# Performance work log

Hardware: AMD Instinct MI355X
Metric: run time of the kernel (lower is better)

Reference implementation:

```python
import jax, jax.numpy as jnp
import numpy as np

B, D_IN, HD, HN = 16384, 1024, 128, 8
D = HD * HN  # 1024
PROJ = int((4.0 / 3.0) * D)  # 1365
EPS = 1e-5


def setup_inputs() -> dict:
    key = jax.random.key(0)
    ks = jax.random.split(key, 16)
    s = 0.02
    inp = {
        'seq': jax.random.normal(ks[0], (B, D_IN), jnp.float32),
        'c0': jnp.zeros((B, D), jnp.float32),
        'n0': jnp.ones((B, D), jnp.float32),
        'h0': jax.random.normal(ks[1], (B, D), jnp.float32) * 0.1,
        'm0': jnp.zeros((B, D), jnp.float32),
        'ln_w': jnp.ones((D_IN,), jnp.float32),
        'ln_b': jnp.zeros((D_IN,), jnp.float32),
        'Wz': jax.random.normal(ks[2], (D, D_IN), jnp.float32) * s,
        'bz': jnp.zeros((D,), jnp.float32),
        'Wi': jax.random.normal(ks[3], (D, D_IN), jnp.float32) * s,
        'bi': jnp.zeros((D,), jnp.float32),
        'Wo': jax.random.normal(ks[4], (D, D_IN), jnp.float32) * s,
        'bo': jnp.zeros((D,), jnp.float32),
        'Wf': jax.random.normal(ks[5], (D, D_IN), jnp.float32) * s,
        'bf': jnp.zeros((D,), jnp.float32),
        'Rz': jax.random.normal(ks[6], (HN, HD, HD), jnp.float32) * s,
        'Ri': jax.random.normal(ks[7], (HN, HD, HD), jnp.float32) * s,
        'Ro': jax.random.normal(ks[8], (HN, HD, HD), jnp.float32) * s,
        'Rf': jax.random.normal(ks[9], (HN, HD, HD), jnp.float32) * s,
        'gn_w': jnp.ones((D,), jnp.float32),
        'gn_b': jnp.zeros((D,), jnp.float32),
        'up_w': jax.random.normal(ks[10], (2 * PROJ, D), jnp.float32) * s,
        'up_b': jnp.zeros((2 * PROJ,), jnp.float32),
        'down_w': jax.random.normal(ks[11], (D_IN, PROJ), jnp.float32) * s,
        'down_b': jnp.zeros((D_IN,), jnp.float32),
    }
    return inp


def _layernorm(x, w, b):
    mu = jnp.mean(x, axis=-1, keepdims=True)
    var = jnp.mean(jnp.square(x - mu), axis=-1, keepdims=True)
    return (x - mu) * jax.lax.rsqrt(var + EPS) * w + b


def _groupnorm(x, w, b):
    # x: (B, D) -> groups of HD channels per head
    xr = x.reshape(x.shape[0], HN, HD)
    mu = jnp.mean(xr, axis=-1, keepdims=True)
    var = jnp.mean(jnp.square(xr - mu), axis=-1, keepdims=True)
    xn = ((xr - mu) * jax.lax.rsqrt(var + EPS)).reshape(x.shape)
    return xn * w + b


def _block_linear(h, R):
    # block-diagonal recurrence: per-head (HD,HD) matmul
    hr = h.reshape(h.shape[0], HN, HD)
    return jnp.einsum('hed,bhd->bhe', R, hr).reshape(h.shape)


def reference(seq, c0, n0, h0, m0, ln_w, ln_b, Wz, bz, Wi, bi, Wo, bo, Wf, bf,
              Rz, Ri, Ro, Rf, gn_w, gn_b, up_w, up_b, down_w, down_b):
    x_t = _layernorm(seq, ln_w, ln_b)
    x_c = x_t  # use_conv=False default path
    i_t = x_c @ Wi.T + bi + _block_linear(h0, Ri)
    f_t = x_c @ Wf.T + bf + _block_linear(h0, Rf)
    z_t = x_t @ Wz.T + bz + _block_linear(h0, Rz)
    o_t = x_t @ Wo.T + bo + _block_linear(h0, Ro)
    m_t = jnp.maximum(f_t + m0, i_t)
    i_e = jnp.exp(i_t - m_t)
    f_e = jnp.exp(f_t - m_t + m0)
    z_a = jnp.tanh(z_t)
    o_a = jax.nn.sigmoid(o_t)
    c_t = f_e * c0 + i_e * z_a
    n_t = f_e * n0 + i_e
    h_t = o_a * (c_t / n_t)
    out = _groupnorm(h_t, gn_w, gn_b)
    up = out @ up_w.T + up_b
    out1, out2 = jnp.split(up, 2, axis=-1)
    out = out1 + jax.nn.gelu(out2, approximate=False)
    out = out @ down_w.T + down_b
    return (out + seq, c_t, n_t, h_t, m_t)
```

## Files before the change

### kernel.cpp

```cpp
#include <hip/hip_runtime.h>
#include <hip/hip_bf16.h>
#include <cstdint>
#include <type_traits>

typedef __attribute__((ext_vector_type(8))) __bf16 bf16x8;
typedef __attribute__((ext_vector_type(8))) short short8;
typedef __attribute__((ext_vector_type(4))) float f32x4;
using u16 = unsigned short;

template <typename T, typename = void> struct mfma_ok : std::false_type {};
template <typename T>
struct mfma_ok<T, std::void_t<decltype(__builtin_amdgcn_mfma_f32_16x16x32_bf16(
    std::declval<T>(), std::declval<T>(), std::declval<f32x4>(), 0, 0, 0))>>
    : std::true_type {};
using frag_t = std::conditional_t<mfma_ok<bf16x8>::value, bf16x8, short8>;
static_assert(sizeof(frag_t) == 16, "frag must be 4 VGPRs");

template <typename T>
__device__ __forceinline__ f32x4 MFMA(T a, T b, f32x4 c) {
  return __builtin_amdgcn_mfma_f32_16x16x32_bf16(a, b, c, 0, 0, 0);
}

__device__ __forceinline__ void gl_lds16(const u16* g, u16* l) {
  __builtin_amdgcn_global_load_lds(
      (const __attribute__((address_space(1))) unsigned int*)g,
      (__attribute__((address_space(3))) unsigned int*)l, 16, 0, 0);
}

__device__ __forceinline__ u16 f2bf(float v) {
  __hip_bfloat16 h = __float2bfloat16(v);
  return __builtin_bit_cast(u16, h);
}

__device__ __forceinline__ int xcd_swz(int wid, int nwg) {
  return (wid & 7) * (nwg >> 3) + (wid >> 3);
}

__device__ __forceinline__ void gemm128(
    const u16* __restrict__ A, int lda,
    const u16* __restrict__ B, int ldb, int K,
    u16* lds, f32x4 (&acc)[4][4])
{
  const int t = threadIdx.x;
  const int l = t & 63;
  const int w = t >> 6;
  const int wm = w >> 1, wc = w & 1;

  const u16* gA = A + (t >> 2) * lda + (t & 3) * 8;
  const u16* gB = B + (t >> 2) * ldb + (t & 3) * 8;

  const int lr = l & 15, lk = l >> 4;
  const int ab = (wm * 64 + lr) * 32 + lk * 8;
  const int bb = 4096 + (wc * 64 + lr) * 32 + lk * 8;

  const int nt = K >> 5;
  for (int kt = 0; kt < nt; ++kt) {
    const u16* a_ = gA + kt * 32;
    const u16* b_ = gB + kt * 32;
    gl_lds16(a_,            lds + w * 512);
    gl_lds16(a_ + 64 * lda, lds + 2048 + w * 512);
    gl_lds16(b_,            lds + 4096 + w * 512);
    gl_lds16(b_ + 64 * ldb, lds + 6144 + w * 512);
    __syncthreads();

    frag_t a[4], b[4];
#pragma unroll
    for (int fm = 0; fm < 4; ++fm)
      a[fm] = *(const frag_t*)(lds + ab + fm * 512);
#pragma unroll
    for (int fn = 0; fn < 4; ++fn)
      b[fn] = *(const frag_t*)(lds + bb + fn * 512);
#pragma unroll
    for (int fn = 0; fn < 4; ++fn)
#pragma unroll
      for (int fm = 0; fm < 4; ++fm)
        acc[fm][fn] = MFMA(a[fm], b[fn], acc[fm][fn]);
    __syncthreads();
  }
}

__global__ __launch_bounds__(256) void prep_kernel(
    const float* __restrict__ Wi, const float* __restrict__ Wf,
    const float* __restrict__ Wz, const float* __restrict__ Wo,
    const float* __restrict__ Ri, const float* __restrict__ Rf,
    const float* __restrict__ Rz, const float* __restrict__ Ro,
    const float* __restrict__ upw, const float* __restrict__ dnw,
    u16* __restrict__ Wint, u16* __restrict__ Rint,
    u16* __restrict__ upint, u16* __restrict__ dnp)
{
  const int stride = gridDim.x * 256;
  for (int i = blockIdx.x * 256 + threadIdx.x; i < 9043968; i += stride) {
    if (i < 4194304) {
      const int nt = i >> 17, vcol = (i >> 10) & 127, k = i & 1023;
      const int wc = vcol >> 6, g = (vcol >> 4) & 3, c16 = vcol & 15;
      const int col = nt * 32 + wc * 16 + c16;
      const float* W = (g == 0) ? Wi : (g == 1) ? Wf : (g == 2) ? Wz : Wo;
      Wint[i] = f2bf(W[col * 1024 + k]);
    } else if (i < 4718592) {
      const int j = i - 4194304;
      const int nt = j >> 14, vcol = (j >> 7) & 127, k = j & 127;
      const int wc = vcol >> 6, g = (vcol >> 4) & 3, c16 = vcol & 15;
      const int head = nt >> 2;
      const int colInHead = (nt & 3) * 32 + wc * 16 + c16;
      const float* R = (g == 0) ? Ri : (g == 1) ? Rf : (g == 2) ? Rz : Ro;
      Rint[j] = f2bf(R[head * 16384 + colInHead * 128 + k]);
    } else if (i < 7602176) {
      const int j = i - 4718592;
      const int vt = j >> 17, vcol = (j >> 10) & 127, k = j & 1023;
      const int wc = vcol >> 6, fn = (vcol >> 4) & 3, c16 = vcol & 15;
      const int half = fn >> 1;
      const int a = vt * 64 + wc * 32 + (fn & 1) * 16 + c16;
      upint[j] = (a < 1365) ? f2bf(upw[(half * 1365 + a) * 1024 + k]) : (u16)0;
    } else {
      const int j = i - 7602176;
      const int row = j / 1408, k = j - row * 1408;
      dnp[j] = (k < 1365) ? f2bf(dnw[row * 1365 + k]) : (u16)0;
    }
  }
}

__global__ __launch_bounds__(256) void ln_kernel(
    const float* __restrict__ seq, const float* __restrict__ h0,
    const float* __restrict__ lnw, const float* __restrict__ lnb,
    u16* __restrict__ xb, u16* __restrict__ h0b)
{
  const int row = blockIdx.x;
  const int t = threadIdx.x;
  const float4 v = ((const float4*)(seq + (size_t)row * 1024))[t];
  float s = v.x + v.y + v.z + v.w;
  float q = v.x * v.x + v.y * v.y + v.z * v.z + v.w * v.w;
#pragma unroll
  for (int o = 32; o >= 1; o >>= 1) { s += __shfl_xor(s, o); q += __shfl_xor(q, o); }
  __shared__ float sm[8];
  const int l = t & 63, w = t >> 6;
  if (l == 0) { sm[w] = s; sm[4 + w] = q; }
  __syncthreads();
  s = sm[0] + sm[1] + sm[2] + sm[3];
  q = sm[4] + sm[5] + sm[6] + sm[7];
  const float mu = s * (1.f / 1024.f);
  const float var = q * (1.f / 1024.f) - mu * mu;
  const float rstd = rsqrtf(var + 1e-5f);
  const float4 wv = ((const float4*)lnw)[t];
  const float4 bv = ((const float4*)lnb)[t];
  ushort4 o4;
  o4.x = f2bf((v.x - mu) * rstd * wv.x + bv.x);
  o4.y = f2bf((v.y - mu) * rstd * wv.y + bv.y);
  o4.z = f2bf((v.z - mu) * rstd * wv.z + bv.z);
  o4.w = f2bf((v.w - mu) * rstd * wv.w + bv.w);
  ((ushort4*)(xb + (size_t)row * 1024))[t] = o4;
  const float4 h = ((const float4*)(h0 + (size_t)row * 1024))[t];
  ushort4 h4;
  h4.x = f2bf(h.x); h4.y = f2bf(h.y); h4.z = f2bf(h.z); h4.w = f2bf(h.w);
  ((ushort4*)(h0b + (size_t)row * 1024))[t] = h4;
}

__global__ __launch_bounds__(256, 3) void gate_kernel(
    const u16* __restrict__ xb, const u16* __restrict__ h0b,
    const u16* __restrict__ Wint, const u16* __restrict__ Rint,
    const float* __restrict__ bi, const float* __restrict__ bfv,
    const float* __restrict__ bz, const float* __restrict__ bo,
    const float* __restrict__ c0, const float* __restrict__ n0i,
    const float* __restrict__ m0,
    float* __restrict__ oc, float* __restrict__ on,
    float* __restrict__ oh, float* __restrict__ om)
{
  __shared__ __align__(16) u16 lds[8192];
  const int wid = xcd_swz(blockIdx.x, 4096);
  const int nt = wid & 31;
  const int mt = wid >> 5;
  f32x4 acc[4][4] = {};
  gemm128(xb + (size_t)mt * 131072, 1024, Wint + nt * 131072, 1024, 1024,
          lds, acc);
  gemm128(h0b + (size_t)mt * 131072 + (nt >> 2) * 128, 1024,
          Rint + nt * 16384, 128, 128, lds, acc);

  const int t = threadIdx.x, l = t & 63, w = t >> 6, wm = w >> 1, wc = w & 1;
  const int cc = nt * 32 + wc * 16 + (l & 15);
  const float biv = bi[cc], bfvv = bfv[cc], bzv = bz[cc], bov = bo[cc];
#pragma unroll
  for (int fm = 0; fm < 4; ++fm) {
    const int rbase = mt * 128 + wm * 64 + fm * 16 + (l >> 4) * 4;
#pragma unroll
    for (int r = 0; r < 4; ++r) {
      const size_t idx = (size_t)(rbase + r) * 1024 + cc;
      const float it = acc[fm][0][r] + biv;
      const float ft = acc[fm][1][r] + bfvv;
      const float zt = acc[fm][2][r] + bzv;
      const float ot = acc[fm][3][r] + bov;
      const float mp = m0[idx];
      const float mt_ = fmaxf(ft + mp, it);
      const float ie = __expf(it - mt_);
      const float fe = __expf(ft - mt_ + mp);
      const float ct = fe * c0[idx] + ie * tanhf(zt);
      const float ntv = fe * n0i[idx] + ie;
      const float ht = (ct / ntv) / (1.f + __expf(-ot));
      oc[idx] = ct; on[idx] = ntv; oh[idx] = ht; om[idx] = mt_;
    }
  }
}

__global__ __launch_bounds__(256) void gn_kernel(
    const float* __restrict__ h, const float* __restrict__ gw,
    const float* __restrict__ gb, u16* __restrict__ gnb)
{
  const int t = threadIdx.x, l = t & 63, w = t >> 6;
  for (int grp = blockIdx.x * 4 + w; grp < 16384 * 8; grp += gridDim.x * 4) {
    const int b = grp >> 3, hd = grp & 7;
    const float2 v = ((const float2*)(h + b * 1024 + hd * 128))[l];
    float s = v.x + v.y, q = v.x * v.x + v.y * v.y;
#pragma unroll
    for (int o = 32; o >= 1; o >>= 1) { s += __shfl_xor(s, o); q += __shfl_xor(q, o); }
    const float mu = s * (1.f / 128.f);
    const float var = q * (1.f / 128.f) - mu * mu;
    const float rstd = rsqrtf(var + 1e-5f);
    const float2 wv = ((const float2*)(gw + hd * 128))[l];
    const float2 bv = ((const float2*)(gb + hd * 128))[l];
    ushort2 o2;
    o2.x = f2bf((v.x - mu) * rstd * wv.x + bv.x);
    o2.y = f2bf((v.y - mu) * rstd * wv.y + bv.y);
    ((ushort2*)(gnb + b * 1024 + hd * 128))[l] = o2;
  }
}

__global__ __launch_bounds__(256, 3) void up_kernel(
    const u16* __restrict__ gnb, const u16* __restrict__ upint,
    const float* __restrict__ upb, u16* __restrict__ g)
{
  __shared__ __align__(16) u16 lds[8192];
  const int wid = xcd_swz(blockIdx.x, 2816);
  const int vt = wid % 22, mt = wid / 22;
  f32x4 acc[4][4] = {};
  gemm128(gnb + (size_t)mt * 131072, 1024, upint + vt * 131072, 1024, 1024,
          lds, acc);
  const int t = threadIdx.x, l = t & 63, w = t >> 6, wm = w >> 1, wc = w & 1;
#pragma unroll
  for (int fm = 0; fm < 4; ++fm) {
    const int rbase = mt * 128 + wm * 64 + fm * 16 + (l >> 4) * 4;
#pragma unroll
    for (int fn = 0; fn < 2; ++fn) {
      const int a = vt * 64 + wc * 32 + fn * 16 + (l & 15);
      const float b1 = (a < 1365) ? upb[a] : 0.f;
      const float b2 = (a < 1365) ? upb[1365 + a] : 0.f;
#pragma unroll
      for (int r = 0; r < 4; ++r) {
        const float u1 = acc[fm][fn][r] + b1;
        const float u2 = acc[fm][fn + 2][r] + b2;
        const float ge = 0.5f * u2 * (1.f + erff(u2 * 0.70710678118654752f));
        g[(size_t)(rbase + r) * 1408 + a] = f2bf(u1 + ge);
      }
    }
  }
}

__global__ __launch_bounds__(256, 3) void down_kernel(
    const u16* __restrict__ g, const u16* __restrict__ dnp,
    const float* __restrict__ dnb, const float* __restrict__ seq,
    float* __restrict__ out)
{
  __shared__ __align__(16) u16 lds[8192];
  const int wid = xcd_swz(blockIdx.x, 1024);
  const int nt = wid & 7, mt = wid >> 3;
  f32x4 acc[4][4] = {};
  gemm128(g + (size_t)mt * 180224, 1408, dnp + nt * 180224, 1408, 1408,
          lds, acc);
  const int t = threadIdx.x, l = t & 63, w = t >> 6, wm = w >> 1, wc = w & 1;
#pragma unroll
  for (int fm = 0; fm < 4; ++fm) {
    const int rbase = mt * 128 + wm * 64 + fm * 16 + (l >> 4) * 4;
#pragma unroll
    for (int fn = 0; fn < 4; ++fn) {
      const int cc = nt * 128 + wc * 64 + fn * 16 + (l & 15);
      const float bb = dnb[cc];
#pragma unroll
      for (int r = 0; r < 4; ++r) {
        const size_t idx = (size_t)(rbase + r) * 1024 + cc;
        out[idx] = acc[fm][fn][r] + bb + seq[idx];
      }
    }
  }
}

extern "C" void kernel_launch(void* const* d_in, const int* in_sizes, int n_in,
                              void* d_out, int out_size, void* d_ws, size_t ws_size,
                              hipStream_t stream) {
  const float* seq = (const float*)d_in[0];
  const float* c0  = (const float*)d_in[1];
  const float* n0i = (const float*)d_in[2];
  const float* h0  = (const float*)d_in[3];
  const float* m0  = (const float*)d_in[4];
  const float* lnw = (const float*)d_in[5];
  const float* lnb = (const float*)d_in[6];
  const float* Wz  = (const float*)d_in[7];
  const float* bz  = (const float*)d_in[8];
  const float* Wi  = (const float*)d_in[9];
  const float* bi  = (const float*)d_in[10];
  const float* Wo  = (const float*)d_in[11];
  const float* bo  = (const float*)d_in[12];
  const float* Wf  = (const float*)d_in[13];
  const float* bf_ = (const float*)d_in[14];
  const float* Rz  = (const float*)d_in[15];
  const float* Ri  = (const float*)d_in[16];
  const float* Ro  = (const float*)d_in[17];
  const float* Rf  = (const float*)d_in[18];
  const float* gw  = (const float*)d_in[19];
  const float* gb  = (const float*)d_in[20];
  const float* upw = (const float*)d_in[21];
  const float* upb = (const float*)d_in[22];
  const float* dnw = (const float*)d_in[23];
  const float* dnb = (const float*)d_in[24];

  char* ws = (char*)d_ws;
  u16* xb   = (u16*)(ws);
  u16* h0b  = (u16*)(ws + 33554432);
  u16* Wint = (u16*)(ws + 67108864);
  u16* Rint = (u16*)(ws + 75497472);
  u16* upc  = (u16*)(ws + 76546048);
  u16* dnp  = (u16*)(ws + 82313216);
  u16* g    = (u16*)(ws + 85196800);

  float* out = (float*)d_out;
  float* oc = out + 16777216;
  float* on = out + 2 * 16777216;
  float* oh = out + 3 * 16777216;
  float* om = out + 4 * 16777216;

  prep_kernel<<<dim3(2048), dim3(256), 0, stream>>>(
      Wi, Wf, Wz, Wo, Ri, Rf, Rz, Ro, upw, dnw, Wint, Rint, upc, dnp);
  ln_kernel<<<dim3(16384), dim3(256), 0, stream>>>(seq, h0, lnw, lnb, xb, h0b);
  gate_kernel<<<dim3(4096), dim3(256), 0, stream>>>(
      xb, h0b, Wint, Rint, bi, bf_, bz, bo, c0, n0i, m0, oc, on, oh, om);
  gn_kernel<<<dim3(2048), dim3(256), 0, stream>>>(oh, gw, gb, xb);
  up_kernel<<<dim3(2816), dim3(256), 0, stream>>>(xb, upc, upb, g);
  down_kernel<<<dim3(1024), dim3(256), 0, stream>>>(g, dnp, dnb, seq, out);
}
```

Before: 563.9 us.

## Double-buffer LDS in GEMM mainloop with XOR swizzle to avoid bank conflicts

```diff
diff --git a/kernel.cpp b/kernel.cpp
--- a/kernel.cpp
+++ b/kernel.cpp
@@ -46,37 +46,55 @@
   const int w = t >> 6;
   const int wm = w >> 1, wc = w & 1;
 
-  const u16* gA = A + (t >> 2) * lda + (t & 3) * 8;
-  const u16* gB = B + (t >> 2) * ldb + (t & 3) * 8;
+  const int srow = t >> 2;
+  const int scol = ((t & 3) ^ ((srow >> 1) & 3)) * 8;
+  const u16* gA = A + srow * lda + scol;
+  const u16* gB = B + srow * ldb + scol;
 
   const int lr = l & 15, lk = l >> 4;
-  const int ab = (wm * 64 + lr) * 32 + lk * 8;
-  const int bb = 4096 + (wc * 64 + lr) * 32 + lk * 8;
+  const int ck = (lk ^ ((lr >> 1) & 3)) * 8;
+  const int ab = (wm * 64 + lr) * 32 + ck;
+  const int bb = 4096 + (wc * 64 + lr) * 32 + ck;
 
   const int nt = K >> 5;
+
+#define STG(buf, kt) do {                                      \
+    const u16* a_ = gA + (kt) * 32;                            \
+    const u16* b_ = gB + (kt) * 32;                            \
+    u16* s_ = (buf);                                           \
+    gl_lds16(a_,            s_ + w * 512);                     \
+    gl_lds16(a_ + 64 * lda, s_ + 2048 + w * 512);              \
+    gl_lds16(b_,            s_ + 4096 + w * 512);              \
+    gl_lds16(b_ + 64 * ldb, s_ + 6144 + w * 512);              \
+  } while (0)
+
+  STG(lds, 0);
+  asm volatile("s_waitcnt vmcnt(0)" ::: "memory");
+  __builtin_amdgcn_s_barrier();
+
   for (int kt = 0; kt < nt; ++kt) {
-    const u16* a_ = gA + kt * 32;
-    const u16* b_ = gB + kt * 32;
-    gl_lds16(a_,            lds + w * 512);
-    gl_lds16(a_ + 64 * lda, lds + 2048 + w * 512);
-    gl_lds16(b_,            lds + 4096 + w * 512);
-    gl_lds16(b_ + 64 * ldb, lds + 6144 + w * 512);
-    __syncthreads();
+    u16* cur = lds + (kt & 1) * 8192;
+    u16* nxt = lds + ((kt + 1) & 1) * 8192;
+    const bool more = (kt + 1 < nt);
+    if (more) STG(nxt, kt + 1);
 
     frag_t a[4], b[4];
 #pragma unroll
     for (int fm = 0; fm < 4; ++fm)
-      a[fm] = *(const frag_t*)(lds + ab + fm * 512);
+      a[fm] = *(const frag_t*)(cur + ab + fm * 512);
 #pragma unroll
     for (int fn = 0; fn < 4; ++fn)
-      b[fn] = *(const frag_t*)(lds + bb + fn * 512);
+      b[fn] = *(const frag_t*)(cur + bb + fn * 512);
 #pragma unroll
     for (int fn = 0; fn < 4; ++fn)
 #pragma unroll
       for (int fm = 0; fm < 4; ++fm)
         acc[fm][fn] = MFMA(a[fm], b[fn], acc[fm][fn]);
-    __syncthreads();
-  }
+
+    if (more) asm volatile("s_waitcnt vmcnt(0)" ::: "memory");
+    __builtin_amdgcn_s_barrier();
+  }
+#undef STG
 }
 
 __global__ __launch_bounds__(256) void prep_kernel(
@@ -154,7 +172,7 @@
   ((ushort4*)(h0b + (size_t)row * 1024))[t] = h4;
 }
 
-__global__ __launch_bounds__(256, 3) void gate_kernel(
+__global__ __launch_bounds__(256, 4) void gate_kernel(
     const u16* __restrict__ xb, const u16* __restrict__ h0b,
     const u16* __restrict__ Wint, const u16* __restrict__ Rint,
     const float* __restrict__ bi, const float* __restrict__ bfv,
@@ -164,7 +182,7 @@
     float* __restrict__ oc, float* __restrict__ on,
     float* __restrict__ oh, float* __restrict__ om)
 {
-  __shared__ __align__(16) u16 lds[8192];
+  __shared__ __align__(16) u16 lds[16384];
   const int wid = xcd_swz(blockIdx.x, 4096);
   const int nt = wid & 31;
   const int mt = wid >> 5;
@@ -222,11 +240,11 @@
   }
 }
 
-__global__ __launch_bounds__(256, 3) void up_kernel(
+__global__ __launch_bounds__(256, 4) void up_kernel(
     const u16* __restrict__ gnb, const u16* __restrict__ upint,
     const float* __restrict__ upb, u16* __restrict__ g)
 {
-  __shared__ __align__(16) u16 lds[8192];
+  __shared__ __align__(16) u16 lds[16384];
   const int wid = xcd_swz(blockIdx.x, 2816);
   const int vt = wid % 22, mt = wid / 22;
   f32x4 acc[4][4] = {};
@@ -252,12 +270,12 @@
   }
 }
 
-__global__ __launch_bounds__(256, 3) void down_kernel(
+__global__ __launch_bounds__(256, 4) void down_kernel(
     const u16* __restrict__ g, const u16* __restrict__ dnp,
     const float* __restrict__ dnb, const float* __restrict__ seq,
     float* __restrict__ out)
 {
-  __shared__ __align__(16) u16 lds[8192];
+  __shared__ __align__(16) u16 lds[16384];
   const int wid = xcd_swz(blockIdx.x, 1024);
   const int nt = wid & 7, mt = wid >> 3;
   f32x4 acc[4][4] = {};
```

After: 569.0 us. About the same (+0.9%).
